# Performance work log

Measured on AMD Instinct MI355X. Metric: run time of the kernel, lower is better.

The kernel has to match this reference:

```python
import jax, jax.numpy as jnp
import numpy as np

D = 128  # hard-coded hidden dim in MLP_T

def setup_inputs() -> dict:
    key = jax.random.key(0)
    ks = jax.random.split(key, 8)
    N, IN = 16384, 768
    return {
        "x": jax.random.normal(ks[0], (N, IN), dtype=jnp.float32),
        "decay_value": 1,
        "W_token": jax.random.normal(ks[1], (IN, D), dtype=jnp.float32) * (IN ** -0.5),
        "b_token": jax.random.normal(ks[2], (D,), dtype=jnp.float32) * 0.02,
        "W_qkv": jax.random.normal(ks[3], (D, 3 * D), dtype=jnp.float32) * (D ** -0.5),
        "b_qkv": jax.random.normal(ks[4], (3 * D,), dtype=jnp.float32) * 0.02,
        "W_fc": jax.random.normal(ks[5], (D, 1), dtype=jnp.float32) * (D ** -0.5),
        "b_fc": jax.random.normal(ks[6], (1,), dtype=jnp.float32) * 0.02,
    }

def reference(x, decay_value, W_token, b_token, W_qkv, b_qkv, W_fc, b_fc):
    # token projection: [N, in_chan] -> [N, 128]
    h = x @ W_token + b_token
    # qkv: [N, 384] split along feature dim into q, k, v of [N, 128]
    qkv = h @ W_qkv + b_qkv
    q, k, v = qkv[:, :D], qkv[:, D:2 * D], qkv[:, 2 * D:]
    # sigmoid attention (no row normalization); dropout is identity in eval mode
    att_scores = jax.nn.sigmoid(q @ k.T)            # [N, N]
    att = att_scores @ v                            # [N, 128]
    out = att @ W_fc + b_fc                         # [N, 1]
    # GradientReversal is identity in the forward pass
    return out
```

## Files before the change

### kernel.cpp

```cpp
#include <hip/hip_runtime.h>
#include <hip/hip_bf16.h>
#include <stdint.h>

#define N_ROWS 16384

typedef __bf16 bf16x8 __attribute__((ext_vector_type(8)));
typedef float f32x4 __attribute__((ext_vector_type(4)));

#define AS1 __attribute__((address_space(1)))
#define AS3 __attribute__((address_space(3)))

#define OFF_WCS  0u
#define OFF_BC   589824u
#define OFF_QB   591360u
#define OFF_KB   4785664u
#define OFF_WV   8979968u
#define OFF_PART 9045504u

__global__ void prep(const float* __restrict__ Wt, const float* __restrict__ Wq,
                     const float* __restrict__ bt, const float* __restrict__ bq,
                     __bf16* __restrict__ WcS, float* __restrict__ bc) {
    int u = blockIdx.x * 256 + threadIdx.x;
    if (u < 768 * 96) {
        int k = u / 96, n4 = u % 96;
        float s[4] = {0, 0, 0, 0};
        const float* wtp = Wt + k * 128;
        const float* wqp = Wq + n4 * 4;
#pragma unroll 8
        for (int d = 0; d < 128; d++) {
            float a = wtp[d];
            float4 b = *(const float4*)(wqp + d * 384);
            s[0] += a * b.x; s[1] += a * b.y; s[2] += a * b.z; s[3] += a * b.w;
        }
        int kb_ = k >> 6, c = (k >> 3) & 7, k7 = k & 7;
#pragma unroll
        for (int j = 0; j < 4; j++) {
            int n = n4 * 4 + j;
            WcS[n * 768 + kb_ * 64 + ((c ^ (n & 7)) << 3) + k7] = (__bf16)s[j];
        }
    }
    if (u < 384) {
        float s = bq[u];
        for (int d = 0; d < 128; d++) s += bt[d] * Wq[d * 384 + u];
        bc[u] = s;
    }
}

__launch_bounds__(256)
__global__ void gemm_qkv(const float* __restrict__ x, const __bf16* __restrict__ WcS,
                         const float* __restrict__ bc, const float* __restrict__ W_fc,
                         __bf16* __restrict__ qb, __bf16* __restrict__ kb,
                         float* __restrict__ wv) {
    __shared__ float  Asm[64 * 64];
    __shared__ __bf16 Bsm[128 * 64];
    __shared__ float  wred[64];
    const int tid = threadIdx.x, wave = tid >> 6, lane = tid & 63;
    const int n16 = lane & 15, q = lane >> 4;
    const int mh = wave >> 1, nw = wave & 1;
    const int row0 = blockIdx.x * 64;
    const int sp = blockIdx.y;

    const char* aptr[4];
    const char* bptr[4];
    {
        int p = (lane & 15) >> 1, half = lane & 1;
#pragma unroll
        for (int i = 0; i < 4; i++) {
            int ar = row0 + wave * 16 + i * 4 + (lane >> 4);
            aptr[i] = (const char*)x + (size_t)ar * 3072 + ((p ^ (ar & 7)) * 8 + half * 4) * 4;
            int br = sp * 128 + wave * 32 + i * 8 + (lane >> 3);
            bptr[i] = (const char*)WcS + (size_t)br * 1536 + (lane & 7) * 16;
        }
    }
    f32x4 acc[2][4];
#pragma unroll
    for (int mt = 0; mt < 2; mt++)
#pragma unroll
        for (int t = 0; t < 4; t++) acc[mt][t] = (f32x4){0, 0, 0, 0};

    for (int kbi = 0; kbi < 12; kbi++) {
#pragma unroll
        for (int i = 0; i < 4; i++)
            __builtin_amdgcn_global_load_lds((const AS1 void*)(aptr[i] + kbi * 256),
                (AS3 void*)((char*)Asm + wave * 4096 + i * 1024), 16, 0, 0);
#pragma unroll
        for (int i = 0; i < 4; i++)
            __builtin_amdgcn_global_load_lds((const AS1 void*)(bptr[i] + kbi * 128),
                (AS3 void*)((char*)Bsm + wave * 4096 + i * 1024), 16, 0, 0);
        __syncthreads();
#pragma unroll
        for (int ks = 0; ks < 2; ks++) {
            const int swz = ((ks * 4 + q) ^ (n16 & 7)) << 3;
            bf16x8 af[2];
#pragma unroll
            for (int mt = 0; mt < 2; mt++) {
                const float* ap = Asm + (mh * 32 + mt * 16 + n16) * 64 + swz;
                f32x4 a0 = *(const f32x4*)ap;
                f32x4 a1 = *(const f32x4*)(ap + 4);
                bf16x8 t;
                t[0] = (__bf16)a0[0]; t[1] = (__bf16)a0[1]; t[2] = (__bf16)a0[2]; t[3] = (__bf16)a0[3];
                t[4] = (__bf16)a1[0]; t[5] = (__bf16)a1[1]; t[6] = (__bf16)a1[2]; t[7] = (__bf16)a1[3];
                af[mt] = t;
            }
#pragma unroll
            for (int t = 0; t < 4; t++) {
                bf16x8 bf = *(const bf16x8*)(Bsm + (nw * 64 + t * 16 + n16) * 64 + swz);
                acc[0][t] = __builtin_amdgcn_mfma_f32_16x16x32_bf16(af[0], bf, acc[0][t], 0, 0, 0);
                acc[1][t] = __builtin_amdgcn_mfma_f32_16x16x32_bf16(af[1], bf, acc[1][t], 0, 0, 0);
            }
        }
        __syncthreads();
    }

    const int clb = nw * 64 + n16;
    if (sp == 0) {
#pragma unroll
        for (int t = 0; t < 4; t++) {
            int cl = clb + t * 16;
            float bcv = bc[cl];
#pragma unroll
            for (int mt = 0; mt < 2; mt++)
#pragma unroll
                for (int r = 0; r < 4; r++) {
                    int row = row0 + mh * 32 + mt * 16 + q * 4 + r;
                    qb[row * 128 + cl] = (__bf16)((acc[mt][t][r] + bcv) * -1.44269504088896f);
                }
        }
    } else if (sp == 1) {
#pragma unroll
        for (int t = 0; t < 4; t++) {
            int d = clb + t * 16;
            float bcv = bc[128 + d];
#pragma unroll
            for (int mt = 0; mt < 2; mt++)
#pragma unroll
                for (int r = 0; r < 4; r++) {
                    int row = row0 + mh * 32 + mt * 16 + q * 4 + r;
                    kb[row * 128 + (((d >> 3) ^ (row & 15)) << 3) + (d & 7)] = (__bf16)(acc[mt][t][r] + bcv);
                }
        }
    } else {
        float wacc[2][4] = {{0, 0, 0, 0}, {0, 0, 0, 0}};
#pragma unroll
        for (int t = 0; t < 4; t++) {
            int cl = clb + t * 16;
            float bcv = bc[256 + cl];
            float wf = W_fc[cl];
#pragma unroll
            for (int mt = 0; mt < 2; mt++)
#pragma unroll
                for (int r = 0; r < 4; r++) wacc[mt][r] += (acc[mt][t][r] + bcv) * wf;
        }
        float vred[2][4];
#pragma unroll
        for (int mt = 0; mt < 2; mt++)
#pragma unroll
            for (int r = 0; r < 4; r++) {
                float v = wacc[mt][r];
                v += __shfl_xor(v, 1, 64);
                v += __shfl_xor(v, 2, 64);
                v += __shfl_xor(v, 4, 64);
                v += __shfl_xor(v, 8, 64);
                vred[mt][r] = v;
                if (nw == 0 && n16 == 0) wred[mh * 32 + mt * 16 + q * 4 + r] = v;
            }
        __syncthreads();
        if (nw == 1 && n16 == 0) {
#pragma unroll
            for (int mt = 0; mt < 2; mt++)
#pragma unroll
                for (int r = 0; r < 4; r++) {
                    int lr = mh * 32 + mt * 16 + q * 4 + r;
                    wv[row0 + lr] = wred[lr] + vred[mt][r];
                }
        }
    }
}

__launch_bounds__(256, 4)
__global__ void attn(const __bf16* __restrict__ qb, const __bf16* __restrict__ kb,
                     const float* __restrict__ wv, float* __restrict__ partial) {
    __shared__ __bf16 kbuf[4 * 32 * 128];
    __shared__ float wlds[2048];
    const int tid = threadIdx.x;
    const int wave = tid >> 6, lane = tid & 63;
    const int n16 = lane & 15, q = lane >> 4;
    const int bid = blockIdx.x;
    const int sp = bid & 7;
    const int rb = bid >> 3;
    const int row0 = rb * 128 + wave * 32;
    const int jb0 = sp * 2048;

    bf16x8 qf[2][4];
#pragma unroll
    for (int mt = 0; mt < 2; mt++)
#pragma unroll
        for (int ks = 0; ks < 4; ks++)
            qf[mt][ks] = *(const bf16x8*)(qb + (size_t)(row0 + mt * 16 + n16) * 128 + ks * 32 + q * 8);
    __builtin_amdgcn_sched_barrier(0);

    {
        const char* wsrc = (const char*)(wv + jb0) + tid * 16;
        char* wdst = (char*)wlds + tid * 16;
        __builtin_amdgcn_global_load_lds((const AS1 void*)wsrc, (AS3 void*)wdst, 16, 0, 0);
        __builtin_amdgcn_global_load_lds((const AS1 void*)(wsrc + 4096),
                                         (AS3 void*)(wdst + 4096), 16, 0, 0);
    }

#define ISSUE(c, slot)                                                                  \
    {                                                                                   \
        const char* gsrc = (const char*)kb + (size_t)(jb0 + (c) * 32) * 256 + wave * 2048; \
        char* gdst = (char*)kbuf + (slot) * 8192 + wave * 2048;                          \
        __builtin_amdgcn_global_load_lds((const AS1 void*)(gsrc + lane * 16),            \
                                         (AS3 void*)gdst, 16, 0, 0);                     \
        __builtin_amdgcn_global_load_lds((const AS1 void*)(gsrc + 1024 + lane * 16),     \
                                         (AS3 void*)(gdst + 1024), 16, 0, 0);            \
    }

    ISSUE(0, 0);
    ISSUE(1, 1);

    float acc[2][4] = {{0}, {0}};

    const __bf16* kaddr[4];
#pragma unroll
    for (int ks = 0; ks < 4; ks++)
        kaddr[ks] = kbuf + n16 * 128 + (((ks * 4 + q) ^ n16) << 3);
    const float* wbase = wlds + n16;

#pragma unroll 4
    for (int jc = 0; jc < 64; jc++) {
        const int jn = (jc + 2 < 64) ? jc + 2 : 63;
        ISSUE(jn, (jc + 2) & 3);

        asm volatile("s_waitcnt vmcnt(4)" ::: "memory");
        __builtin_amdgcn_sched_barrier(0);
        __builtin_amdgcn_s_barrier();

        const int slot = jc & 3;
#pragma unroll
        for (int t = 0; t < 2; t++) {
            f32x4 s0 = (f32x4){0, 0, 0, 0}, s1 = (f32x4){0, 0, 0, 0};
            __builtin_amdgcn_s_setprio(1);
#pragma unroll
            for (int ks = 0; ks < 4; ks++) {
                bf16x8 bf = *(const bf16x8*)(kaddr[ks] + slot * 4096 + t * 2048);
                s0 = __builtin_amdgcn_mfma_f32_16x16x32_bf16(qf[0][ks], bf, s0, 0, 0, 0);
                s1 = __builtin_amdgcn_mfma_f32_16x16x32_bf16(qf[1][ks], bf, s1, 0, 0, 0);
            }
            __builtin_amdgcn_s_setprio(0);
            const float wval = wbase[jc * 32 + t * 16];
#pragma unroll
            for (int r = 0; r < 4; r++) {
                acc[0][r] += __builtin_amdgcn_rcpf(1.0f + __builtin_amdgcn_exp2f(s0[r])) * wval;
                acc[1][r] += __builtin_amdgcn_rcpf(1.0f + __builtin_amdgcn_exp2f(s1[r])) * wval;
            }
        }
    }
#undef ISSUE

#pragma unroll
    for (int mt = 0; mt < 2; mt++)
#pragma unroll
        for (int r = 0; r < 4; r++) {
            float v = acc[mt][r];
            v += __shfl_xor(v, 1, 64);
            v += __shfl_xor(v, 2, 64);
            v += __shfl_xor(v, 4, 64);
            v += __shfl_xor(v, 8, 64);
            if (n16 == 0) partial[sp * N_ROWS + row0 + mt * 16 + q * 4 + r] = v;
        }
}

__global__ void reduce_out(const float* __restrict__ partial, const float* __restrict__ b_fc,
                           float* __restrict__ out) {
    int i = blockIdx.x * 256 + threadIdx.x;
    float v = b_fc[0];
#pragma unroll
    for (int s = 0; s < 8; s++) v += partial[s * N_ROWS + i];
    out[i] = v;
}

extern "C" void kernel_launch(void* const* d_in, const int* in_sizes, int n_in,
                              void* d_out, int out_size, void* d_ws, size_t ws_size,
                              hipStream_t stream) {
    const float* x       = (const float*)d_in[0];
    const float* W_token = (const float*)d_in[2];
    const float* b_token = (const float*)d_in[3];
    const float* W_qkv   = (const float*)d_in[4];
    const float* b_qkv   = (const float*)d_in[5];
    const float* W_fc    = (const float*)d_in[6];
    const float* b_fc    = (const float*)d_in[7];
    float* out = (float*)d_out;
    char* ws = (char*)d_ws;

    __bf16* WcS = (__bf16*)(ws + OFF_WCS);
    float*  bc  = (float*)(ws + OFF_BC);
    __bf16* qb  = (__bf16*)(ws + OFF_QB);
    __bf16* kb  = (__bf16*)(ws + OFF_KB);
    float*  wv  = (float*)(ws + OFF_WV);
    float*  part = (float*)(ws + OFF_PART);

    prep<<<288, 256, 0, stream>>>(W_token, W_qkv, b_token, b_qkv, WcS, bc);
    gemm_qkv<<<dim3(256, 3), 256, 0, stream>>>(x, WcS, bc, W_fc, qb, kb, wv);
    attn<<<1024, 256, 0, stream>>>(qb, kb, wv, part);
    reduce_out<<<64, 256, 0, stream>>>(part, b_fc, out);
}
```

Measured before the change: 202.9 us.

## Fuse qkv split into one gemm block and software-pipeline sigmoid in attention

The qkv GEMM now computes all 384 output columns per 64-row block, so x is read once rather than three times. The block keeps 24 accumulators per wave and a larger LDS buffer for B. In the attention loop, the sigmoid and weighted accumulation for each score tile are deferred by one step, with a final drain after the loop. This lets the exp/rcp work overlap with the next tile's MFMAs. The costs are higher register and LDS pressure in the GEMM and fewer GEMM blocks (256 instead of 768), which reduces parallelism.

```diff
diff --git a/kernel.cpp b/kernel.cpp
--- a/kernel.cpp
+++ b/kernel.cpp
@@ -52,31 +52,28 @@
                          __bf16* __restrict__ qb, __bf16* __restrict__ kb,
                          float* __restrict__ wv) {
     __shared__ float  Asm[64 * 64];
-    __shared__ __bf16 Bsm[128 * 64];
-    __shared__ float  wred[64];
+    __shared__ __bf16 Bsm[384 * 64];
     const int tid = threadIdx.x, wave = tid >> 6, lane = tid & 63;
     const int n16 = lane & 15, q = lane >> 4;
     const int mh = wave >> 1, nw = wave & 1;
     const int row0 = blockIdx.x * 64;
-    const int sp = blockIdx.y;
 
     const char* aptr[4];
-    const char* bptr[4];
     {
         int p = (lane & 15) >> 1, half = lane & 1;
 #pragma unroll
         for (int i = 0; i < 4; i++) {
             int ar = row0 + wave * 16 + i * 4 + (lane >> 4);
             aptr[i] = (const char*)x + (size_t)ar * 3072 + ((p ^ (ar & 7)) * 8 + half * 4) * 4;
-            int br = sp * 128 + wave * 32 + i * 8 + (lane >> 3);
-            bptr[i] = (const char*)WcS + (size_t)br * 1536 + (lane & 7) * 16;
-        }
-    }
-    f32x4 acc[2][4];
+        }
+    }
+    const char* bptr0 = (const char*)WcS + (size_t)(wave * 96 + (lane >> 3)) * 1536 + (lane & 7) * 16;
+
+    f32x4 acc[2][12];
 #pragma unroll
     for (int mt = 0; mt < 2; mt++)
 #pragma unroll
-        for (int t = 0; t < 4; t++) acc[mt][t] = (f32x4){0, 0, 0, 0};
+        for (int t = 0; t < 12; t++) acc[mt][t] = (f32x4){0, 0, 0, 0};
 
     for (int kbi = 0; kbi < 12; kbi++) {
 #pragma unroll
@@ -84,9 +81,9 @@
             __builtin_amdgcn_global_load_lds((const AS1 void*)(aptr[i] + kbi * 256),
                 (AS3 void*)((char*)Asm + wave * 4096 + i * 1024), 16, 0, 0);
 #pragma unroll
-        for (int i = 0; i < 4; i++)
-            __builtin_amdgcn_global_load_lds((const AS1 void*)(bptr[i] + kbi * 128),
-                (AS3 void*)((char*)Bsm + wave * 4096 + i * 1024), 16, 0, 0);
+        for (int i = 0; i < 12; i++)
+            __builtin_amdgcn_global_load_lds((const AS1 void*)(bptr0 + i * 12288 + kbi * 128),
+                (AS3 void*)((char*)Bsm + wave * 12288 + i * 1024), 16, 0, 0);
         __syncthreads();
 #pragma unroll
         for (int ks = 0; ks < 2; ks++) {
@@ -103,8 +100,8 @@
                 af[mt] = t;
             }
 #pragma unroll
-            for (int t = 0; t < 4; t++) {
-                bf16x8 bf = *(const bf16x8*)(Bsm + (nw * 64 + t * 16 + n16) * 64 + swz);
+            for (int t = 0; t < 12; t++) {
+                bf16x8 bf = *(const bf16x8*)(Bsm + (nw * 192 + t * 16 + n16) * 64 + swz);
                 acc[0][t] = __builtin_amdgcn_mfma_f32_16x16x32_bf16(af[0], bf, acc[0][t], 0, 0, 0);
                 acc[1][t] = __builtin_amdgcn_mfma_f32_16x16x32_bf16(af[1], bf, acc[1][t], 0, 0, 0);
             }
@@ -112,12 +109,12 @@
         __syncthreads();
     }
 
-    const int clb = nw * 64 + n16;
-    if (sp == 0) {
-#pragma unroll
-        for (int t = 0; t < 4; t++) {
-            int cl = clb + t * 16;
-            float bcv = bc[cl];
+    float wacc[2][4] = {{0, 0, 0, 0}, {0, 0, 0, 0}};
+#pragma unroll
+    for (int t = 0; t < 12; t++) {
+        const int cl = nw * 192 + t * 16 + n16;
+        const float bcv = bc[cl];
+        if (cl < 128) {
 #pragma unroll
             for (int mt = 0; mt < 2; mt++)
 #pragma unroll
@@ -125,12 +122,8 @@
                     int row = row0 + mh * 32 + mt * 16 + q * 4 + r;
                     qb[row * 128 + cl] = (__bf16)((acc[mt][t][r] + bcv) * -1.44269504088896f);
                 }
-        }
-    } else if (sp == 1) {
-#pragma unroll
-        for (int t = 0; t < 4; t++) {
-            int d = clb + t * 16;
-            float bcv = bc[128 + d];
+        } else if (cl < 256) {
+            const int d = cl - 128;
 #pragma unroll
             for (int mt = 0; mt < 2; mt++)
 #pragma unroll
@@ -138,20 +131,15 @@
                     int row = row0 + mh * 32 + mt * 16 + q * 4 + r;
                     kb[row * 128 + (((d >> 3) ^ (row & 15)) << 3) + (d & 7)] = (__bf16)(acc[mt][t][r] + bcv);
                 }
-        }
-    } else {
-        float wacc[2][4] = {{0, 0, 0, 0}, {0, 0, 0, 0}};
-#pragma unroll
-        for (int t = 0; t < 4; t++) {
-            int cl = clb + t * 16;
-            float bcv = bc[256 + cl];
-            float wf = W_fc[cl];
+        } else {
+            const float wf = W_fc[cl - 256];
 #pragma unroll
             for (int mt = 0; mt < 2; mt++)
 #pragma unroll
                 for (int r = 0; r < 4; r++) wacc[mt][r] += (acc[mt][t][r] + bcv) * wf;
         }
-        float vred[2][4];
+    }
+    if (nw == 1) {
 #pragma unroll
         for (int mt = 0; mt < 2; mt++)
 #pragma unroll
@@ -161,19 +149,8 @@
                 v += __shfl_xor(v, 2, 64);
                 v += __shfl_xor(v, 4, 64);
                 v += __shfl_xor(v, 8, 64);
-                vred[mt][r] = v;
-                if (nw == 0 && n16 == 0) wred[mh * 32 + mt * 16 + q * 4 + r] = v;
-            }
-        __syncthreads();
-        if (nw == 1 && n16 == 0) {
-#pragma unroll
-            for (int mt = 0; mt < 2; mt++)
-#pragma unroll
-                for (int r = 0; r < 4; r++) {
-                    int lr = mh * 32 + mt * 16 + q * 4 + r;
-                    wv[row0 + lr] = wred[lr] + vred[mt][r];
-                }
-        }
+                if (n16 == 0) wv[row0 + mh * 32 + mt * 16 + q * 4 + r] = v;
+            }
     }
 }
 
@@ -221,6 +198,8 @@
     ISSUE(1, 1);
 
     float acc[2][4] = {{0}, {0}};
+    f32x4 ps0 = (f32x4){0, 0, 0, 0}, ps1 = (f32x4){0, 0, 0, 0};
+    float pw = 0.0f;
 
     const __bf16* kaddr[4];
 #pragma unroll
@@ -249,15 +228,22 @@
                 s1 = __builtin_amdgcn_mfma_f32_16x16x32_bf16(qf[1][ks], bf, s1, 0, 0, 0);
             }
             __builtin_amdgcn_s_setprio(0);
-            const float wval = wbase[jc * 32 + t * 16];
 #pragma unroll
             for (int r = 0; r < 4; r++) {
-                acc[0][r] += __builtin_amdgcn_rcpf(1.0f + __builtin_amdgcn_exp2f(s0[r])) * wval;
-                acc[1][r] += __builtin_amdgcn_rcpf(1.0f + __builtin_amdgcn_exp2f(s1[r])) * wval;
-            }
+                acc[0][r] += __builtin_amdgcn_rcpf(1.0f + __builtin_amdgcn_exp2f(ps0[r])) * pw;
+                acc[1][r] += __builtin_amdgcn_rcpf(1.0f + __builtin_amdgcn_exp2f(ps1[r])) * pw;
+            }
+            ps0 = s0; ps1 = s1;
+            pw = wbase[jc * 32 + t * 16];
         }
     }
 #undef ISSUE
+
+#pragma unroll
+    for (int r = 0; r < 4; r++) {
+        acc[0][r] += __builtin_amdgcn_rcpf(1.0f + __builtin_amdgcn_exp2f(ps0[r])) * pw;
+        acc[1][r] += __builtin_amdgcn_rcpf(1.0f + __builtin_amdgcn_exp2f(ps1[r])) * pw;
+    }
 
 #pragma unroll
     for (int mt = 0; mt < 2; mt++)
@@ -302,7 +288,7 @@
     float*  part = (float*)(ws + OFF_PART);
 
     prep<<<288, 256, 0, stream>>>(W_token, W_qkv, b_token, b_qkv, WcS, bc);
-    gemm_qkv<<<dim3(256, 3), 256, 0, stream>>>(x, WcS, bc, W_fc, qb, kb, wv);
+    gemm_qkv<<<256, 256, 0, stream>>>(x, WcS, bc, W_fc, qb, kb, wv);
     attn<<<1024, 256, 0, stream>>>(qb, kb, wv, part);
     reduce_out<<<64, 256, 0, stream>>>(part, b_fc, out);
 }
```

Result: slower. 215.8 us (+6.3%).

## Pre-convert x to bf16 in prep, widen GEMM K-tile, software-pipeline sigmoid in attention

Applied to the files above, without the earlier changes.

The prep kernel gains 6144 extra blocks that convert x to swizzled bf16 in workspace. gemm_qkv then loads bf16 A tiles straight into LDS with a 128-wide K step, which halves its K iterations and drops the per-iteration fp32-to-bf16 conversion. Separately, the attention loop defers the exp/rcp sigmoid epilogue of each score tile by one step, so the transcendental work can overlap the next tile's MFMAs. The cost is an extra full pass over x (read fp32, write bf16) plus larger LDS tiles in the GEMM.

```diff
diff --git a/kernel.cpp b/kernel.cpp
--- a/kernel.cpp
+++ b/kernel.cpp
@@ -16,11 +16,26 @@
 #define OFF_KB   4785664u
 #define OFF_WV   8979968u
 #define OFF_PART 9045504u
-
-__global__ void prep(const float* __restrict__ Wt, const float* __restrict__ Wq,
-                     const float* __restrict__ bt, const float* __restrict__ bq,
+#define OFF_XB   9569792u
+
+__global__ void prep(const float* __restrict__ x, const float* __restrict__ Wt,
+                     const float* __restrict__ Wq, const float* __restrict__ bt,
+                     const float* __restrict__ bq, __bf16* __restrict__ xb,
                      __bf16* __restrict__ WcS, float* __restrict__ bc) {
-    int u = blockIdx.x * 256 + threadIdx.x;
+    if (blockIdx.x < 6144) {
+        int cid = blockIdx.x * 256 + threadIdx.x;
+        int r = cid / 96, cc = cid - r * 96;
+        int g = cc >> 4, c = cc & 15;
+        const float* src = x + (size_t)r * 768 + cc * 8;
+        float4 a = *(const float4*)src;
+        float4 b = *(const float4*)(src + 4);
+        bf16x8 o;
+        o[0] = (__bf16)a.x; o[1] = (__bf16)a.y; o[2] = (__bf16)a.z; o[3] = (__bf16)a.w;
+        o[4] = (__bf16)b.x; o[5] = (__bf16)b.y; o[6] = (__bf16)b.z; o[7] = (__bf16)b.w;
+        *(bf16x8*)(xb + (size_t)r * 768 + g * 128 + ((c ^ (r & 15)) << 3)) = o;
+        return;
+    }
+    int u = (blockIdx.x - 6144) * 256 + threadIdx.x;
     if (u < 768 * 96) {
         int k = u / 96, n4 = u % 96;
         float s[4] = {0, 0, 0, 0};
@@ -32,11 +47,11 @@
             float4 b = *(const float4*)(wqp + d * 384);
             s[0] += a * b.x; s[1] += a * b.y; s[2] += a * b.z; s[3] += a * b.w;
         }
-        int kb_ = k >> 6, c = (k >> 3) & 7, k7 = k & 7;
+        int kg = k >> 7, c = (k >> 3) & 15, k7 = k & 7;
 #pragma unroll
         for (int j = 0; j < 4; j++) {
             int n = n4 * 4 + j;
-            WcS[n * 768 + kb_ * 64 + ((c ^ (n & 7)) << 3) + k7] = (__bf16)s[j];
+            WcS[n * 768 + kg * 128 + ((c ^ (n & 15)) << 3) + k7] = (__bf16)s[j];
         }
     }
     if (u < 384) {
@@ -47,12 +62,12 @@
 }
 
 __launch_bounds__(256)
-__global__ void gemm_qkv(const float* __restrict__ x, const __bf16* __restrict__ WcS,
+__global__ void gemm_qkv(const __bf16* __restrict__ xb, const __bf16* __restrict__ WcS,
                          const float* __restrict__ bc, const float* __restrict__ W_fc,
                          __bf16* __restrict__ qb, __bf16* __restrict__ kb,
                          float* __restrict__ wv) {
-    __shared__ float  Asm[64 * 64];
-    __shared__ __bf16 Bsm[128 * 64];
+    __shared__ __bf16 Asm[64 * 128];
+    __shared__ __bf16 Bsm[128 * 128];
     __shared__ float  wred[64];
     const int tid = threadIdx.x, wave = tid >> 6, lane = tid & 63;
     const int n16 = lane & 15, q = lane >> 4;
@@ -61,52 +76,49 @@
     const int sp = blockIdx.y;
 
     const char* aptr[4];
-    const char* bptr[4];
-    {
-        int p = (lane & 15) >> 1, half = lane & 1;
-#pragma unroll
-        for (int i = 0; i < 4; i++) {
-            int ar = row0 + wave * 16 + i * 4 + (lane >> 4);
-            aptr[i] = (const char*)x + (size_t)ar * 3072 + ((p ^ (ar & 7)) * 8 + half * 4) * 4;
-            int br = sp * 128 + wave * 32 + i * 8 + (lane >> 3);
-            bptr[i] = (const char*)WcS + (size_t)br * 1536 + (lane & 7) * 16;
-        }
-    }
+    const char* bptr[8];
+#pragma unroll
+    for (int i = 0; i < 4; i++) {
+        int ar = row0 + wave * 16 + i * 4 + (lane >> 4);
+        aptr[i] = (const char*)xb + (size_t)ar * 1536 + (lane & 15) * 16;
+    }
+#pragma unroll
+    for (int i = 0; i < 8; i++) {
+        int br = sp * 128 + wave * 32 + i * 4 + (lane >> 4);
+        bptr[i] = (const char*)WcS + (size_t)br * 1536 + (lane & 15) * 16;
+    }
+
     f32x4 acc[2][4];
 #pragma unroll
     for (int mt = 0; mt < 2; mt++)
 #pragma unroll
         for (int t = 0; t < 4; t++) acc[mt][t] = (f32x4){0, 0, 0, 0};
 
-    for (int kbi = 0; kbi < 12; kbi++) {
+    const char* aP = (const char*)Asm + mh * 8192 + n16 * 256;
+    const char* bP = (const char*)Bsm + nw * 16384 + n16 * 256;
+    int swz[4];
+#pragma unroll
+    for (int ks = 0; ks < 4; ks++) swz[ks] = ((ks * 4 + q) ^ n16) << 4;
+
+    for (int kbi = 0; kbi < 6; kbi++) {
 #pragma unroll
         for (int i = 0; i < 4; i++)
             __builtin_amdgcn_global_load_lds((const AS1 void*)(aptr[i] + kbi * 256),
                 (AS3 void*)((char*)Asm + wave * 4096 + i * 1024), 16, 0, 0);
 #pragma unroll
-        for (int i = 0; i < 4; i++)
-            __builtin_amdgcn_global_load_lds((const AS1 void*)(bptr[i] + kbi * 128),
-                (AS3 void*)((char*)Bsm + wave * 4096 + i * 1024), 16, 0, 0);
+        for (int i = 0; i < 8; i++)
+            __builtin_amdgcn_global_load_lds((const AS1 void*)(bptr[i] + kbi * 256),
+                (AS3 void*)((char*)Bsm + wave * 8192 + i * 1024), 16, 0, 0);
         __syncthreads();
 #pragma unroll
-        for (int ks = 0; ks < 2; ks++) {
-            const int swz = ((ks * 4 + q) ^ (n16 & 7)) << 3;
-            bf16x8 af[2];
-#pragma unroll
-            for (int mt = 0; mt < 2; mt++) {
-                const float* ap = Asm + (mh * 32 + mt * 16 + n16) * 64 + swz;
-                f32x4 a0 = *(const f32x4*)ap;
-                f32x4 a1 = *(const f32x4*)(ap + 4);
-                bf16x8 t;
-                t[0] = (__bf16)a0[0]; t[1] = (__bf16)a0[1]; t[2] = (__bf16)a0[2]; t[3] = (__bf16)a0[3];
-                t[4] = (__bf16)a1[0]; t[5] = (__bf16)a1[1]; t[6] = (__bf16)a1[2]; t[7] = (__bf16)a1[3];
-                af[mt] = t;
-            }
+        for (int ks = 0; ks < 4; ks++) {
+            bf16x8 af0 = *(const bf16x8*)(aP + swz[ks]);
+            bf16x8 af1 = *(const bf16x8*)(aP + 4096 + swz[ks]);
 #pragma unroll
             for (int t = 0; t < 4; t++) {
-                bf16x8 bf = *(const bf16x8*)(Bsm + (nw * 64 + t * 16 + n16) * 64 + swz);
-                acc[0][t] = __builtin_amdgcn_mfma_f32_16x16x32_bf16(af[0], bf, acc[0][t], 0, 0, 0);
-                acc[1][t] = __builtin_amdgcn_mfma_f32_16x16x32_bf16(af[1], bf, acc[1][t], 0, 0, 0);
+                bf16x8 bf = *(const bf16x8*)(bP + t * 4096 + swz[ks]);
+                acc[0][t] = __builtin_amdgcn_mfma_f32_16x16x32_bf16(af0, bf, acc[0][t], 0, 0, 0);
+                acc[1][t] = __builtin_amdgcn_mfma_f32_16x16x32_bf16(af1, bf, acc[1][t], 0, 0, 0);
             }
         }
         __syncthreads();
@@ -221,6 +233,8 @@
     ISSUE(1, 1);
 
     float acc[2][4] = {{0}, {0}};
+    f32x4 ps0 = (f32x4){0, 0, 0, 0}, ps1 = (f32x4){0, 0, 0, 0};
+    float pw = 0.0f;
 
     const __bf16* kaddr[4];
 #pragma unroll
@@ -249,15 +263,22 @@
                 s1 = __builtin_amdgcn_mfma_f32_16x16x32_bf16(qf[1][ks], bf, s1, 0, 0, 0);
             }
             __builtin_amdgcn_s_setprio(0);
-            const float wval = wbase[jc * 32 + t * 16];
 #pragma unroll
             for (int r = 0; r < 4; r++) {
-                acc[0][r] += __builtin_amdgcn_rcpf(1.0f + __builtin_amdgcn_exp2f(s0[r])) * wval;
-                acc[1][r] += __builtin_amdgcn_rcpf(1.0f + __builtin_amdgcn_exp2f(s1[r])) * wval;
+                acc[0][r] += __builtin_amdgcn_rcpf(1.0f + __builtin_amdgcn_exp2f(ps0[r])) * pw;
+                acc[1][r] += __builtin_amdgcn_rcpf(1.0f + __builtin_amdgcn_exp2f(ps1[r])) * pw;
             }
+            ps0 = s0; ps1 = s1;
+            pw = wbase[jc * 32 + t * 16];
         }
     }
 #undef ISSUE
+
+#pragma unroll
+    for (int r = 0; r < 4; r++) {
+        acc[0][r] += __builtin_amdgcn_rcpf(1.0f + __builtin_amdgcn_exp2f(ps0[r])) * pw;
+        acc[1][r] += __builtin_amdgcn_rcpf(1.0f + __builtin_amdgcn_exp2f(ps1[r])) * pw;
+    }
 
 #pragma unroll
     for (int mt = 0; mt < 2; mt++)
@@ -300,9 +321,10 @@
     __bf16* kb  = (__bf16*)(ws + OFF_KB);
     float*  wv  = (float*)(ws + OFF_WV);
     float*  part = (float*)(ws + OFF_PART);
-
-    prep<<<288, 256, 0, stream>>>(W_token, W_qkv, b_token, b_qkv, WcS, bc);
-    gemm_qkv<<<dim3(256, 3), 256, 0, stream>>>(x, WcS, bc, W_fc, qb, kb, wv);
+    __bf16* xb  = (__bf16*)(ws + OFF_XB);
+
+    prep<<<6432, 256, 0, stream>>>(x, W_token, W_qkv, b_token, b_qkv, xb, WcS, bc);
+    gemm_qkv<<<dim3(256, 3), 256, 0, stream>>>(xb, WcS, bc, W_fc, qb, kb, wv);
     attn<<<1024, 256, 0, stream>>>(qb, kb, wv, part);
     reduce_out<<<64, 256, 0, stream>>>(part, b_fc, out);
 }
```

Result: slower. 218.2 us (+7.5%).
